# Kernel tuning notes

Hardware: AMD Instinct MI355X
Metric: run time of the kernel (lower is better)

Reference implementation:

```python
import jax, jax.numpy as jnp
import numpy as np

SIZE = (2, 2)


def setup_inputs() -> dict:
    key = jax.random.key(0)
    k1, k2 = jax.random.split(key)
    B, H, W, C = 32, 64, 64, 128
    out_flat = (H * SIZE[0]) * (W * SIZE[1]) * C  # 2,097,152
    updates = jax.random.normal(k1, (B, H, W, C), dtype=jnp.float32)
    mask = jax.random.randint(k2, (B, H, W, C), 0, out_flat, dtype=jnp.int32)
    return {"updates": updates, "mask": mask}


def reference(updates, mask):
    B, H, W, C = updates.shape
    outH, outW = H * SIZE[0], W * SIZE[1]
    flat = outH * outW * C
    # batch index broadcast to match mask, then flat scatter (tf.scatter_nd sums duplicates)
    b = jnp.broadcast_to(jnp.arange(B, dtype=jnp.int32)[:, None, None, None], mask.shape)
    ret = jnp.zeros((B, flat), dtype=updates.dtype)
    ret = ret.at[b.reshape(-1), mask.reshape(-1)].add(updates.reshape(-1))
    return ret.reshape(B, outH, outW, C)
```

## Files before the change

kernel.cpp:

```cpp
#include <hip/hip_runtime.h>


constexpr int B = 32;
constexpr int IN_PER_B = 1 << 19;
constexpr int OUT_PER_B = 1 << 21;
constexpr int N = B * IN_PER_B;
constexpr int OUT_N = B * OUT_PER_B;

constexpr int BKT_BITS = 13;
constexpr int BKT_SIZE = 1 << BKT_BITS;
constexpr int NBKT = B * (OUT_PER_B >> BKT_BITS);
constexpr int CAP = 3072;
constexpr int CHUNK = 4096;
constexpr int P1_BLOCKS = N / CHUNK;
constexpr size_t BINS_BYTES = (size_t)NBKT * CAP * 4ull;
constexpr size_t CNT_BYTES = (size_t)NBKT * 4ull;
constexpr size_t WS_NEEDED = BINS_BYTES + CNT_BYTES;

__device__ __forceinline__ unsigned pack_val19(float v) {
  unsigned bits = __float_as_uint(v);
  return (bits + 0x1000u) >> 13;
}
__device__ __forceinline__ float unpack_val19(unsigned p) {
  return __uint_as_float((p & 0x7FFFFu) << 13);
}

__global__ __launch_bounds__(256) void p1_bin(const int4* __restrict__ msk,
                                              const float4* __restrict__ upd,
                                              unsigned* __restrict__ bins,
                                              int* __restrict__ cnt) {
  __shared__ int hist[256];
  __shared__ int scan[256];
  __shared__ int lstart[256];
  __shared__ int adj[256];
  __shared__ unsigned spair[CHUNK];
  __shared__ unsigned char sbkt[CHUNK];

  const int t = threadIdx.x;
  const int blk = blockIdx.x;
  const int b = blk >> 7;
  const long chunk4 = (long)blk * (CHUNK / 4);

  hist[t] = 0;
  __syncthreads();

  int4 m[4];
  float4 u[4];
  int rank[16];
#pragma unroll
  for (int k = 0; k < 4; k++) {
    m[k] = msk[chunk4 + k * 256 + t];
    u[k] = upd[chunk4 + k * 256 + t];
  }
#pragma unroll
  for (int k = 0; k < 4; k++) {
    int idx[4] = {m[k].x, m[k].y, m[k].z, m[k].w};
#pragma unroll
    for (int c = 0; c < 4; c++) {
      int bkt = idx[c] >> BKT_BITS;
      rank[k * 4 + c] = atomicAdd(&hist[bkt], 1);
    }
  }
  __syncthreads();

  scan[t] = hist[t];
  __syncthreads();
  for (int off = 1; off < 256; off <<= 1) {
    int v = (t >= off) ? scan[t - off] : 0;
    __syncthreads();
    scan[t] += v;
    __syncthreads();
  }
  const int ls = scan[t] - hist[t];
  lstart[t] = ls;
  const int gb = (b << 8) + t;
  int cbase = (hist[t] > 0) ? atomicAdd(&cnt[gb], hist[t]) : 0;
  adj[t] = cbase - ls;
  __syncthreads();

#pragma unroll
  for (int k = 0; k < 4; k++) {
    int idx[4] = {m[k].x, m[k].y, m[k].z, m[k].w};
    float val[4] = {u[k].x, u[k].y, u[k].z, u[k].w};
#pragma unroll
    for (int c = 0; c < 4; c++) {
      int bkt = idx[c] >> BKT_BITS;
      int pos = lstart[bkt] + rank[k * 4 + c];
      spair[pos] = ((unsigned)(idx[c] & (BKT_SIZE - 1)) << 19) | pack_val19(val[c]);
      sbkt[pos] = (unsigned char)bkt;
    }
  }
  __syncthreads();

#pragma unroll
  for (int k = 0; k < 16; k++) {
    int j = k * 256 + t;
    int bkt = sbkt[j];
    int slot = adj[bkt] + j;
    if (slot < CAP) {
      bins[((long)((b << 8) + bkt)) * CAP + slot] = spair[j];
    }
  }
}

__global__ __launch_bounds__(256) void p2_acc(const unsigned* __restrict__ bins,
                                              const int* __restrict__ cnt,
                                              float4* __restrict__ out) {
  __shared__ float acc[BKT_SIZE];
  const int t = threadIdx.x;
  const int gb = blockIdx.x;

#pragma unroll
  for (int k = 0; k < BKT_SIZE / 256; k++) acc[k * 256 + t] = 0.f;
  __syncthreads();

  int count = cnt[gb];
  if (count > CAP) count = CAP;
  const long base = (long)gb * CAP;

  int nv = count >> 2;
  const uint4* bins4 = (const uint4*)(bins + base);
  for (int p = t; p < nv; p += 256) {
    uint4 pr = bins4[p];
    atomicAdd(&acc[pr.x >> 19], unpack_val19(pr.x));
    atomicAdd(&acc[pr.y >> 19], unpack_val19(pr.y));
    atomicAdd(&acc[pr.z >> 19], unpack_val19(pr.z));
    atomicAdd(&acc[pr.w >> 19], unpack_val19(pr.w));
  }
  for (int p = (nv << 2) + t; p < count; p += 256) {
    unsigned pr = bins[base + p];
    atomicAdd(&acc[pr >> 19], unpack_val19(pr));
  }
  __syncthreads();

  const long ob4 = (long)gb * (BKT_SIZE / 4);
#pragma unroll
  for (int k = 0; k < BKT_SIZE / 1024; k++) {
    int i = k * 256 + t;
    out[ob4 + i] = make_float4(acc[i * 4], acc[i * 4 + 1], acc[i * 4 + 2], acc[i * 4 + 3]);
  }
}

__global__ __launch_bounds__(256) void zero_kernel(float4* __restrict__ out) {
  int i = blockIdx.x * 256 + threadIdx.x;
  out[i] = make_float4(0.f, 0.f, 0.f, 0.f);
}

__global__ __launch_bounds__(256) void scatter_atomic(const float4* __restrict__ upd,
                                                      const int4* __restrict__ msk,
                                                      float* __restrict__ out) {
  int i = blockIdx.x * 256 + threadIdx.x;
  int4 m = msk[i];
  float4 u = upd[i];
  int b = i >> 17;
  float* outb = out + (long)b * OUT_PER_B;
  unsafeAtomicAdd(outb + m.x, u.x);
  unsafeAtomicAdd(outb + m.y, u.y);
  unsafeAtomicAdd(outb + m.z, u.z);
  unsafeAtomicAdd(outb + m.w, u.w);
}

extern "C" void kernel_launch(void* const* d_in, const int* in_sizes, int n_in,
                              void* d_out, int out_size, void* d_ws, size_t ws_size,
                              hipStream_t stream) {
  const float4* upd = (const float4*)d_in[0];
  const int4* msk = (const int4*)d_in[1];

  if (ws_size >= WS_NEEDED) {
    unsigned* bins = (unsigned*)d_ws;
    int* cnt = (int*)((char*)d_ws + BINS_BYTES);
    hipMemsetAsync(cnt, 0, CNT_BYTES, stream);
    p1_bin<<<P1_BLOCKS, 256, 0, stream>>>(msk, upd, bins, cnt);
    p2_acc<<<NBKT, 256, 0, stream>>>(bins, cnt, (float4*)d_out);
  } else {
    zero_kernel<<<OUT_N / 4 / 256, 256, 0, stream>>>((float4*)d_out);
    scatter_atomic<<<N / 4 / 256, 256, 0, stream>>>(upd, msk, (float*)d_out);
  }
}
```

Baseline: 451.6 us.

## Restructure binning and accumulation kernels with wave-shuffle scan and precomputed destinations

The binning kernel moves to 512 threads per block and replaces the shared-memory Hillis-Steele scan, which needed many barriers, with a wave shuffle scan plus a cross-wave fixup. Each element's global destination index is precomputed and stored next to its packed value, and overflow entries are sent to a dump slot, so the final store loop no longer does branches or per-bucket lookups. The accumulation kernel issues its bin loads before zeroing shared memory so load latency overlaps the zeroing, and it writes its output with nontemporal stores. This costs more shared memory per block (uint2 per element), and the unrolled accumulation assumes count never exceeds CAP (3072 = 3*256*4), which the existing clamp guarantees.

New measurement: 429.7 us. 1.05x faster.

```diff
diff --git a/kernel.cpp b/kernel.cpp
--- a/kernel.cpp
+++ b/kernel.cpp
@@ -1,5 +1,7 @@
 #include <hip/hip_runtime.h>
 
+
+typedef float f32x4 __attribute__((ext_vector_type(4)));
 
 constexpr int B = 32;
 constexpr int IN_PER_B = 1 << 19;
@@ -12,8 +14,10 @@
 constexpr int NBKT = B * (OUT_PER_B >> BKT_BITS);
 constexpr int CAP = 3072;
 constexpr int CHUNK = 4096;
+constexpr int P1_THREADS = 512;
 constexpr int P1_BLOCKS = N / CHUNK;
-constexpr size_t BINS_BYTES = (size_t)NBKT * CAP * 4ull;
+constexpr unsigned DUMP_IDX = (unsigned)NBKT * (unsigned)CAP;
+constexpr size_t BINS_BYTES = ((size_t)NBKT * CAP + 16) * 4ull;
 constexpr size_t CNT_BYTES = (size_t)NBKT * 4ull;
 constexpr size_t WS_NEEDED = BINS_BYTES + CNT_BYTES;
 
@@ -25,119 +29,151 @@
   return __uint_as_float((p & 0x7FFFFu) << 13);
 }
 
-__global__ __launch_bounds__(256) void p1_bin(const int4* __restrict__ msk,
-                                              const float4* __restrict__ upd,
-                                              unsigned* __restrict__ bins,
-                                              int* __restrict__ cnt) {
+__global__ __launch_bounds__(P1_THREADS) void p1_bin(const int4* __restrict__ msk,
+                                                     const float4* __restrict__ upd,
+                                                     unsigned* __restrict__ bins,
+                                                     int* __restrict__ cnt) {
   __shared__ int hist[256];
-  __shared__ int scan[256];
-  __shared__ int lstart[256];
-  __shared__ int adj[256];
-  __shared__ unsigned spair[CHUNK];
-  __shared__ unsigned char sbkt[CHUNK];
+  __shared__ int wsum[4];
+  __shared__ unsigned adjg[256];
+  __shared__ unsigned lsthr[256];
+  __shared__ uint2 sdata[CHUNK];
 
   const int t = threadIdx.x;
   const int blk = blockIdx.x;
   const int b = blk >> 7;
-  const long chunk4 = (long)blk * (CHUNK / 4);
-
-  hist[t] = 0;
-  __syncthreads();
-
-  int4 m[4];
-  float4 u[4];
-  int rank[16];
-#pragma unroll
-  for (int k = 0; k < 4; k++) {
-    m[k] = msk[chunk4 + k * 256 + t];
-    u[k] = upd[chunk4 + k * 256 + t];
-  }
-#pragma unroll
-  for (int k = 0; k < 4; k++) {
+  const long c4 = (long)blk * (CHUNK / 4);
+
+  if (t < 256) hist[t] = 0;
+
+  int4 m[2];
+  float4 u[2];
+#pragma unroll
+  for (int k = 0; k < 2; k++) {
+    m[k] = msk[c4 + k * P1_THREADS + t];
+    u[k] = upd[c4 + k * P1_THREADS + t];
+  }
+  __syncthreads();
+
+  int rank[8];
+#pragma unroll
+  for (int k = 0; k < 2; k++) {
     int idx[4] = {m[k].x, m[k].y, m[k].z, m[k].w};
 #pragma unroll
-    for (int c = 0; c < 4; c++) {
-      int bkt = idx[c] >> BKT_BITS;
-      rank[k * 4 + c] = atomicAdd(&hist[bkt], 1);
+    for (int c = 0; c < 4; c++)
+      rank[k * 4 + c] = atomicAdd(&hist[idx[c] >> BKT_BITS], 1);
+  }
+  __syncthreads();
+
+  int h = 0, v = 0;
+  if (t < 256) {
+    h = hist[t];
+    v = h;
+#pragma unroll
+    for (int off = 1; off < 64; off <<= 1) {
+      int pv = __shfl_up(v, off);
+      if ((t & 63) >= off) v += pv;
     }
-  }
-  __syncthreads();
-
-  scan[t] = hist[t];
-  __syncthreads();
-  for (int off = 1; off < 256; off <<= 1) {
-    int v = (t >= off) ? scan[t - off] : 0;
-    __syncthreads();
-    scan[t] += v;
-    __syncthreads();
-  }
-  const int ls = scan[t] - hist[t];
-  lstart[t] = ls;
-  const int gb = (b << 8) + t;
-  int cbase = (hist[t] > 0) ? atomicAdd(&cnt[gb], hist[t]) : 0;
-  adj[t] = cbase - ls;
-  __syncthreads();
-
-#pragma unroll
-  for (int k = 0; k < 4; k++) {
+    if ((t & 63) == 63) wsum[t >> 6] = v;
+  }
+  __syncthreads();
+  if (t < 256) {
+    const int w = t >> 6;
+    int pre = 0;
+    if (w > 0) pre += wsum[0];
+    if (w > 1) pre += wsum[1];
+    if (w > 2) pre += wsum[2];
+    const int ls = pre + v - h;
+    const int gb = (b << 8) + t;
+    const int cbase = (h > 0) ? atomicAdd(&cnt[gb], h) : 0;
+    adjg[t] = (unsigned)gb * (unsigned)CAP + (unsigned)(cbase - ls);
+    int thr = CAP - cbase;
+    thr = thr < 0 ? 0 : (thr > 0xFFFF ? 0xFFFF : thr);
+    lsthr[t] = (unsigned)ls | ((unsigned)thr << 16);
+  }
+  __syncthreads();
+
+#pragma unroll
+  for (int k = 0; k < 2; k++) {
     int idx[4] = {m[k].x, m[k].y, m[k].z, m[k].w};
     float val[4] = {u[k].x, u[k].y, u[k].z, u[k].w};
 #pragma unroll
     for (int c = 0; c < 4; c++) {
-      int bkt = idx[c] >> BKT_BITS;
-      int pos = lstart[bkt] + rank[k * 4 + c];
-      spair[pos] = ((unsigned)(idx[c] & (BKT_SIZE - 1)) << 19) | pack_val19(val[c]);
-      sbkt[pos] = (unsigned char)bkt;
+      const int bkt = idx[c] >> BKT_BITS;
+      const unsigned lt = lsthr[bkt];
+      const int r = rank[k * 4 + c];
+      const int pos = (int)(lt & 0xFFFFu) + r;
+      unsigned g = adjg[bkt] + (unsigned)pos;
+      if ((unsigned)r >= (lt >> 16)) g = DUMP_IDX;
+      const unsigned pair =
+          ((unsigned)(idx[c] & (BKT_SIZE - 1)) << 19) | pack_val19(val[c]);
+      sdata[pos] = make_uint2(pair, g);
     }
   }
   __syncthreads();
 
 #pragma unroll
-  for (int k = 0; k < 16; k++) {
-    int j = k * 256 + t;
-    int bkt = sbkt[j];
-    int slot = adj[bkt] + j;
-    if (slot < CAP) {
-      bins[((long)((b << 8) + bkt)) * CAP + slot] = spair[j];
-    }
+  for (int k = 0; k < CHUNK / P1_THREADS; k++) {
+    uint2 e = sdata[k * P1_THREADS + t];
+    bins[e.y] = e.x;
   }
 }
 
 __global__ __launch_bounds__(256) void p2_acc(const unsigned* __restrict__ bins,
                                               const int* __restrict__ cnt,
-                                              float4* __restrict__ out) {
+                                              f32x4* __restrict__ out) {
   __shared__ float acc[BKT_SIZE];
   const int t = threadIdx.x;
   const int gb = blockIdx.x;
 
-#pragma unroll
-  for (int k = 0; k < BKT_SIZE / 256; k++) acc[k * 256 + t] = 0.f;
-  __syncthreads();
-
   int count = cnt[gb];
   if (count > CAP) count = CAP;
   const long base = (long)gb * CAP;
-
-  int nv = count >> 2;
-  const uint4* bins4 = (const uint4*)(bins + base);
-  for (int p = t; p < nv; p += 256) {
-    uint4 pr = bins4[p];
-    atomicAdd(&acc[pr.x >> 19], unpack_val19(pr.x));
-    atomicAdd(&acc[pr.y >> 19], unpack_val19(pr.y));
-    atomicAdd(&acc[pr.z >> 19], unpack_val19(pr.z));
-    atomicAdd(&acc[pr.w >> 19], unpack_val19(pr.w));
-  }
-  for (int p = (nv << 2) + t; p < count; p += 256) {
-    unsigned pr = bins[base + p];
-    atomicAdd(&acc[pr >> 19], unpack_val19(pr));
-  }
+  const uint4* b4 = (const uint4*)(bins + base);
+  const int nv = count >> 2;
+
+  uint4 v0 = make_uint4(0, 0, 0, 0), v1 = v0, v2 = v0;
+  const bool h0 = t < nv, h1 = t + 256 < nv, h2 = t + 512 < nv;
+  if (h0) v0 = b4[t];
+  if (h1) v1 = b4[t + 256];
+  if (h2) v2 = b4[t + 512];
+  const int rem = count - (nv << 2);
+  unsigned tv = 0;
+  const bool ht = t < rem;
+  if (ht) tv = bins[base + (nv << 2) + t];
+
+  f32x4* a4 = (f32x4*)acc;
+#pragma unroll
+  for (int k = 0; k < BKT_SIZE / 4 / 256; k++)
+    a4[k * 256 + t] = (f32x4){0.f, 0.f, 0.f, 0.f};
+  __syncthreads();
+
+  if (h0) {
+    atomicAdd(&acc[v0.x >> 19], unpack_val19(v0.x));
+    atomicAdd(&acc[v0.y >> 19], unpack_val19(v0.y));
+    atomicAdd(&acc[v0.z >> 19], unpack_val19(v0.z));
+    atomicAdd(&acc[v0.w >> 19], unpack_val19(v0.w));
+  }
+  if (h1) {
+    atomicAdd(&acc[v1.x >> 19], unpack_val19(v1.x));
+    atomicAdd(&acc[v1.y >> 19], unpack_val19(v1.y));
+    atomicAdd(&acc[v1.z >> 19], unpack_val19(v1.z));
+    atomicAdd(&acc[v1.w >> 19], unpack_val19(v1.w));
+  }
+  if (h2) {
+    atomicAdd(&acc[v2.x >> 19], unpack_val19(v2.x));
+    atomicAdd(&acc[v2.y >> 19], unpack_val19(v2.y));
+    atomicAdd(&acc[v2.z >> 19], unpack_val19(v2.z));
+    atomicAdd(&acc[v2.w >> 19], unpack_val19(v2.w));
+  }
+  if (ht) atomicAdd(&acc[tv >> 19], unpack_val19(tv));
   __syncthreads();
 
   const long ob4 = (long)gb * (BKT_SIZE / 4);
 #pragma unroll
-  for (int k = 0; k < BKT_SIZE / 1024; k++) {
-    int i = k * 256 + t;
-    out[ob4 + i] = make_float4(acc[i * 4], acc[i * 4 + 1], acc[i * 4 + 2], acc[i * 4 + 3]);
+  for (int k = 0; k < BKT_SIZE / 4 / 256; k++) {
+    f32x4 o = a4[k * 256 + t];
+    __builtin_nontemporal_store(o, &out[ob4 + k * 256 + t]);
   }
 }
 
@@ -169,9 +205,9 @@
   if (ws_size >= WS_NEEDED) {
     unsigned* bins = (unsigned*)d_ws;
     int* cnt = (int*)((char*)d_ws + BINS_BYTES);
-    hipMemsetAsync(cnt, 0, CNT_BYTES, stream);
-    p1_bin<<<P1_BLOCKS, 256, 0, stream>>>(msk, upd, bins, cnt);
-    p2_acc<<<NBKT, 256, 0, stream>>>(bins, cnt, (float4*)d_out);
+    (void)hipMemsetAsync(cnt, 0, CNT_BYTES, stream);
+    p1_bin<<<P1_BLOCKS, P1_THREADS, 0, stream>>>(msk, upd, bins, cnt);
+    p2_acc<<<NBKT, 256, 0, stream>>>(bins, cnt, (f32x4*)d_out);
   } else {
     zero_kernel<<<OUT_N / 4 / 256, 256, 0, stream>>>((float4*)d_out);
     scatter_atomic<<<N / 4 / 256, 256, 0, stream>>>(upd, msk, (float*)d_out);
```
